# Optimization experiments

Hardware: AMD Instinct MI355X
Metric: run time of the kernel (lower is better)

The kernel has to match this reference:

```python
import jax, jax.numpy as jnp
import numpy as np

N_NODES = 50000
N_EDGES = 500000
D = 128
K_CLUSTERS = 1024  # fixed cluster count for Kongming_Cluster
EPS = 1e-8


def setup_inputs() -> dict:
    key = jax.random.key(0)
    k1, k2, k3, k4 = jax.random.split(key, 4)
    x = jax.random.normal(k1, (N_NODES, D), dtype=jnp.float32)
    edge_index = jax.random.randint(k2, (2, N_EDGES), 0, N_NODES, dtype=jnp.int32)
    W1 = jax.random.normal(k3, (D, D), dtype=jnp.float32) * (1.0 / np.sqrt(D))
    b1 = jax.random.normal(k4, (D,), dtype=jnp.float32) * 0.01
    return {"x": x, "edge_index": edge_index, "W1": W1, "b1": b1}


def reference(x, edge_index, W1, b1):
    src, dst = edge_index[0], edge_index[1]
    # --- SLPropagate: mean aggregation of neighbor features over edge list ---
    msg = x[src]                                               # [E, D] gather
    agg = jax.ops.segment_sum(msg, dst, num_segments=N_NODES)  # [N, D] scatter-add
    deg = jax.ops.segment_sum(jnp.ones((N_EDGES,), x.dtype), dst, num_segments=N_NODES)
    h = agg / jnp.maximum(deg, 1.0)[:, None]                   # [N, D]

    # --- Kongming_Cluster: cosine-similarity assignment to K centroids ---
    hn = h / (jnp.linalg.norm(h, axis=-1, keepdims=True) + EPS)  # row-normalized
    centroids = hn[:K_CLUSTERS]                                  # [K, D]
    sim = hn @ centroids.T                                       # [N, K] cosine sims
    assign = jnp.argmax(sim, axis=-1)                            # [N] cluster index
    counts = jax.ops.segment_sum(jnp.ones((N_NODES,), x.dtype), assign,
                                 num_segments=K_CLUSTERS)
    xc = jax.ops.segment_sum(h, assign, num_segments=K_CLUSTERS)
    xc = xc / jnp.maximum(counts, 1.0)[:, None]                  # [K, D] cluster means

    # --- lin1 on compressed representation ---
    y = xc @ W1.T + b1                                           # [K, D]

    # --- Kongming_Reconstruct: scatter/gather back to per-node rows ---
    out = y[assign]                                              # [N, D]
    return out
```

## Files before the change

### kernel.cpp

```cpp
#include <hip/hip_runtime.h>

#define N_NODES 50000
#define N_EDGES 500000
#define DIM 128
#define KC 1024
#define CAP 64
#define EPSV 1e-8f
#define LO_SCALE 4096.0f
#define INV_LO_SCALE (1.0f / 4096.0f)

typedef _Float16 f16x8 __attribute__((ext_vector_type(8)));
typedef _Float16 f16x2 __attribute__((ext_vector_type(2)));
typedef float f32x4 __attribute__((ext_vector_type(4)));

__global__ void fill_buckets_k(const int* __restrict__ ei, int* __restrict__ bucket,
                               int* __restrict__ cursor) {
    int e = blockIdx.x * blockDim.x + threadIdx.x;
    if (e >= N_EDGES) return;
    int src = ei[e];
    int dst = ei[N_EDGES + e];
    int pos = atomicAdd(cursor + dst, 1);
    if (pos < CAP) bucket[dst * CAP + pos] = src;
}

__global__ void agg_norm_k(const float* __restrict__ x, const int* __restrict__ bucket,
                           const int* __restrict__ cursor, float* __restrict__ h,
                           _Float16* __restrict__ Ahi, _Float16* __restrict__ Alo) {
    int lane = threadIdx.x & 63;
    int wv = threadIdx.x >> 6;
    int n = blockIdx.x * 4 + wv;

    int cnt = cursor[n];
    if (cnt > CAP) cnt = CAP;
    int v = (lane < cnt) ? bucket[n * CAP + lane] : 0x7fffffff;

#pragma unroll
    for (int k = 2; k <= 64; k <<= 1) {
#pragma unroll
        for (int j = k >> 1; j >= 1; j >>= 1) {
            int other = __shfl_xor(v, j);
            bool lower = ((lane & j) == 0);
            bool asc = ((lane & k) == 0);
            int mn = min(v, other), mx = max(v, other);
            v = (lower == asc) ? mn : mx;
        }
    }

    const float2* x2 = (const float2*)x;
    float ax = 0.f, ay = 0.f;
    for (int j = 0; j < cnt; ++j) {
        int s = __shfl(v, j);
        float2 t = x2[(size_t)s * 64 + lane];
        ax += t.x; ay += t.y;
    }
    float degf = (float)(cnt > 0 ? cnt : 1);
    float hx = ax / degf, hy = ay / degf;

    float ss = hx * hx + hy * hy;
#pragma unroll
    for (int o = 1; o < 64; o <<= 1) ss += __shfl_xor(ss, o);
    float denom = sqrtf(ss) + EPSV;
    float hnx = hx / denom, hny = hy / denom;

    ((float2*)h)[(size_t)n * 64 + lane] = make_float2(hx, hy);

    _Float16 hix = (_Float16)hnx, hiy = (_Float16)hny;
    _Float16 lox = (_Float16)((hnx - (float)hix) * LO_SCALE);
    _Float16 loy = (_Float16)((hny - (float)hiy) * LO_SCALE);
    f16x2 ph; ph[0] = hix; ph[1] = hiy;
    f16x2 pl; pl[0] = lox; pl[1] = loy;
    *(f16x2*)(Ahi + (size_t)n * DIM + lane * 2) = ph;
    *(f16x2*)(Alo + (size_t)n * DIM + lane * 2) = pl;
}

#define SWZ14(u) ((u) ^ ((((u) >> 8) & 7) << 4))

__global__ __launch_bounds__(256, 3) void sim_mfma3_k(const _Float16* __restrict__ Ahi,
                                                      const _Float16* __restrict__ Alo,
                                                      int* __restrict__ assign) {
    __shared__ __align__(16) char Bs[2][16384];
    const int lane = threadIdx.x & 63;
    const int wv = threadIdx.x >> 6;
    const int r16 = lane & 15, kg = lane >> 4;
    const int m0 = blockIdx.x * 128 + wv * 32;

    int ar0 = m0 + r16;      if (ar0 > N_NODES - 1) ar0 = N_NODES - 1;
    int ar1 = m0 + 16 + r16; if (ar1 > N_NODES - 1) ar1 = N_NODES - 1;
    f16x8 ah0[4], al0[4], ah1[4], al1[4];
#pragma unroll
    for (int ks = 0; ks < 4; ++ks) {
        size_t o0 = (size_t)ar0 * DIM + ks * 32 + kg * 8;
        size_t o1 = (size_t)ar1 * DIM + ks * 32 + kg * 8;
        ah0[ks] = *(const f16x8*)(Ahi + o0);
        al0[ks] = *(const f16x8*)(Alo + o0);
        ah1[ks] = *(const f16x8*)(Ahi + o1);
        al1[ks] = *(const f16x8*)(Alo + o1);
    }

    const int u0 = wv * 2048 + lane * 16;
    const int u1 = u0 + 1024;
    const int d0 = SWZ14(u0), d1 = SWZ14(u1);
    const int e0 = u0 >> 1, e1 = u1 >> 1;

    float best0_0 = -1e30f, best0_1 = -1e30f, best0_2 = -1e30f, best0_3 = -1e30f;
    float best1_0 = -1e30f, best1_1 = -1e30f, best1_2 = -1e30f, best1_3 = -1e30f;
    int bi0_0 = 0, bi0_1 = 0, bi0_2 = 0, bi0_3 = 0;
    int bi1_0 = 0, bi1_1 = 0, bi1_2 = 0, bi1_3 = 0;

    const int rbase = r16 * 256;
    const int x4 = (r16 & 7) << 4;

    f16x8 sA = *(const f16x8*)(Ahi + e0);
    f16x8 sB = *(const f16x8*)(Ahi + e1);
    f16x8 sC = *(const f16x8*)(Alo + e0);
    f16x8 sD = *(const f16x8*)(Alo + e1);
    {
        char* bc = &Bs[0][0];
        *(f16x8*)(bc + d0) = sA; *(f16x8*)(bc + d1) = sB;
        *(f16x8*)(bc + 8192 + d0) = sC; *(f16x8*)(bc + 8192 + d1) = sD;
    }
    __syncthreads();

    for (int kc = 0; kc < 32; ++kc) {
        const int cur = kc & 1;
        if (kc < 31) {
            int go = (kc + 1) * 4096;
            sA = *(const f16x8*)(Ahi + go + e0);
            sB = *(const f16x8*)(Ahi + go + e1);
            sC = *(const f16x8*)(Alo + go + e0);
            sD = *(const f16x8*)(Alo + go + e1);
        }
        char* bc = &Bs[cur][0];
#pragma unroll
        for (int ns = 0; ns < 2; ++ns) {
            f32x4 c1a = (f32x4){0.f, 0.f, 0.f, 0.f};
            f32x4 c2a = (f32x4){0.f, 0.f, 0.f, 0.f};
            f32x4 c1b = (f32x4){0.f, 0.f, 0.f, 0.f};
            f32x4 c2b = (f32x4){0.f, 0.f, 0.f, 0.f};
#pragma unroll
            for (int ks = 0; ks < 4; ++ks) {
                int off = ns * 4096 + rbase + ((ks * 64 + kg * 16) ^ x4);
                f16x8 bh = *(const f16x8*)(bc + off);
                f16x8 bl = *(const f16x8*)(bc + 8192 + off);
                c1a = __builtin_amdgcn_mfma_f32_16x16x32_f16(ah0[ks], bh, c1a, 0, 0, 0);
                c2a = __builtin_amdgcn_mfma_f32_16x16x32_f16(ah0[ks], bl, c2a, 0, 0, 0);
                c2a = __builtin_amdgcn_mfma_f32_16x16x32_f16(al0[ks], bh, c2a, 0, 0, 0);
                c1b = __builtin_amdgcn_mfma_f32_16x16x32_f16(ah1[ks], bh, c1b, 0, 0, 0);
                c2b = __builtin_amdgcn_mfma_f32_16x16x32_f16(ah1[ks], bl, c2b, 0, 0, 0);
                c2b = __builtin_amdgcn_mfma_f32_16x16x32_f16(al1[ks], bh, c2b, 0, 0, 0);
            }
            int col = kc * 32 + ns * 16 + r16;
            float s;
            s = c1a[0] + c2a[0] * INV_LO_SCALE; if (s > best0_0) { best0_0 = s; bi0_0 = col; }
            s = c1a[1] + c2a[1] * INV_LO_SCALE; if (s > best0_1) { best0_1 = s; bi0_1 = col; }
            s = c1a[2] + c2a[2] * INV_LO_SCALE; if (s > best0_2) { best0_2 = s; bi0_2 = col; }
            s = c1a[3] + c2a[3] * INV_LO_SCALE; if (s > best0_3) { best0_3 = s; bi0_3 = col; }
            s = c1b[0] + c2b[0] * INV_LO_SCALE; if (s > best1_0) { best1_0 = s; bi1_0 = col; }
            s = c1b[1] + c2b[1] * INV_LO_SCALE; if (s > best1_1) { best1_1 = s; bi1_1 = col; }
            s = c1b[2] + c2b[2] * INV_LO_SCALE; if (s > best1_2) { best1_2 = s; bi1_2 = col; }
            s = c1b[3] + c2b[3] * INV_LO_SCALE; if (s > best1_3) { best1_3 = s; bi1_3 = col; }
        }
        if (kc < 31) {
            char* bn = &Bs[cur ^ 1][0];
            *(f16x8*)(bn + d0) = sA; *(f16x8*)(bn + d1) = sB;
            *(f16x8*)(bn + 8192 + d0) = sC; *(f16x8*)(bn + 8192 + d1) = sD;
        }
        __syncthreads();
    }

    float bestA[8] = {best0_0, best0_1, best0_2, best0_3,
                      best1_0, best1_1, best1_2, best1_3};
    int bidxA[8] = {bi0_0, bi0_1, bi0_2, bi0_3, bi1_0, bi1_1, bi1_2, bi1_3};
#pragma unroll
    for (int q = 0; q < 8; ++q) {
        float b = bestA[q];
        int bi = bidxA[q];
#pragma unroll
        for (int o = 1; o < 16; o <<= 1) {
            float os = __shfl_xor(b, o);
            int oi = __shfl_xor(bi, o);
            if (os > b || (os == b && oi < bi)) { b = os; bi = oi; }
        }
        if (r16 == 0) {
            int gr = m0 + (q >> 2) * 16 + kg * 4 + (q & 3);
            if (gr < N_NODES) assign[gr] = bi;
        }
    }
}

__global__ void cluster_count_k(const int* __restrict__ assign, int* __restrict__ counts) {
    int n = blockIdx.x * 256 + threadIdx.x;
    if (n < N_NODES) atomicAdd(counts + assign[n], 1);
}

__global__ void scan_k(const int* __restrict__ counts, int* __restrict__ offs,
                       int* __restrict__ ccur) {
    __shared__ int buf[KC];
    int t = threadIdx.x;
    int v = counts[t];
    buf[t] = v;
    __syncthreads();
#pragma unroll
    for (int o = 1; o < KC; o <<= 1) {
        int u = (t >= o) ? buf[t - o] : 0;
        __syncthreads();
        buf[t] += u;
        __syncthreads();
    }
    int excl = buf[t] - v;
    offs[t] = excl;
    ccur[t] = excl;
}

__global__ void fill_clist_k(const int* __restrict__ assign, int* __restrict__ ccur,
                             int* __restrict__ clist) {
    int n = blockIdx.x * 256 + threadIdx.x;
    if (n >= N_NODES) return;
    int p = atomicAdd(ccur + assign[n], 1);
    clist[p] = n;
}

__global__ void xc_sum_k(const float* __restrict__ h, const int* __restrict__ clist,
                         const int* __restrict__ offs, const int* __restrict__ counts,
                         float* __restrict__ xc) {
    int c = blockIdx.x, t = threadIdx.x;
    int s = offs[c], cnt = counts[c];
    float acc = 0.f;
    for (int i = 0; i < cnt; ++i) {
        int n = clist[s + i];
        acc += h[(size_t)n * DIM + t];
    }
    xc[c * DIM + t] = acc;
}

__global__ void y_gemm_k(const float* __restrict__ xc, const int* __restrict__ counts,
                         const float* __restrict__ W1, const float* __restrict__ b1,
                         float* __restrict__ y) {
    __shared__ float xr[DIM];
    int c = blockIdx.x, t = threadIdx.x;
    int cnt = counts[c];
    float cntf = (float)(cnt > 0 ? cnt : 1);
    xr[t] = xc[c * DIM + t] / cntf;
    __syncthreads();

    const float4* w4 = (const float4*)(W1 + t * DIM);
    float a0 = 0.f, a1 = 0.f, a2 = 0.f, a3 = 0.f;
#pragma unroll
    for (int kk = 0; kk < 32; ++kk) {
        float4 w = w4[kk];
        a0 = fmaf(xr[4 * kk + 0], w.x, a0);
        a1 = fmaf(xr[4 * kk + 1], w.y, a1);
        a2 = fmaf(xr[4 * kk + 2], w.z, a2);
        a3 = fmaf(xr[4 * kk + 3], w.w, a3);
    }
    y[c * DIM + t] = (a0 + a1) + (a2 + a3) + b1[t];
}

__global__ void scatter_out_k(const float* __restrict__ y, const int* __restrict__ assign,
                              float* __restrict__ out) {
    int i = blockIdx.x * blockDim.x + threadIdx.x;
    int n = i >> 5, q = i & 31;
    int a = assign[n];
    ((float4*)out)[(size_t)n * 32 + q] = ((const float4*)y)[a * 32 + q];
}

extern "C" void kernel_launch(void* const* d_in, const int* in_sizes, int n_in,
                              void* d_out, int out_size, void* d_ws, size_t ws_size,
                              hipStream_t stream) {
    const float* x  = (const float*)d_in[0];
    const int*   ei = (const int*)d_in[1];
    const float* W1 = (const float*)d_in[2];
    const float* b1 = (const float*)d_in[3];
    float* out = (float*)d_out;

    char* ws = (char*)d_ws;
    float* h      = (float*)(ws);
    int*   bucket = (int*)(ws + 25600000);
    int*   clist  = (int*)(ws + 25600000);
    int*   offs   = (int*)(ws + 25800000);
    int*   ccur   = (int*)(ws + 25804096);
    int*   cursor = (int*)(ws + 38400000);
    int*   counts = (int*)(ws + 38600000);
    float* xc     = (float*)(ws + 38604096);
    int*   assign = (int*)(ws + 39128384);
    float* y      = (float*)(ws + 39328384);

    _Float16* Ahi = (_Float16*)d_out;
    _Float16* Alo = (_Float16*)((char*)d_out + 12800000);

    hipMemsetAsync(ws + 38400000, 0, 204096, stream);

    fill_buckets_k<<<(N_EDGES + 255) / 256, 256, 0, stream>>>(ei, bucket, cursor);
    agg_norm_k<<<N_NODES / 4, 256, 0, stream>>>(x, bucket, cursor, h, Ahi, Alo);
    sim_mfma3_k<<<(N_NODES + 127) / 128, 256, 0, stream>>>(Ahi, Alo, assign);
    cluster_count_k<<<(N_NODES + 255) / 256, 256, 0, stream>>>(assign, counts);
    scan_k<<<1, KC, 0, stream>>>(counts, offs, ccur);
    fill_clist_k<<<(N_NODES + 255) / 256, 256, 0, stream>>>(assign, ccur, clist);
    xc_sum_k<<<KC, 128, 0, stream>>>(h, clist, offs, counts, xc);
    y_gemm_k<<<KC, 128, 0, stream>>>(xc, counts, W1, b1, y);
    scatter_out_k<<<(N_NODES * 32) / 256, 256, 0, stream>>>(y, assign, out);
}
```

Baseline: 195.7 us.

## Process two nodes per wave in aggregation and fuse cluster counting and GEMM kernels

The aggregation kernel now handles two nodes per wavefront, with 32 lanes each loading float4 rows, whenever both degrees are at most 32. It falls back to the old one-node-per-wave path otherwise. Cluster counting is folded into the similarity kernel's argmax epilogue as atomics, and the cluster-sum and lin1 GEMM kernels are merged into one. This removes two kernel launches and one global xc round trip, and improves lane use for the typical degree of about 10. In exchange it adds a divergent fallback branch and atomic contention on the counts array.

```diff
diff --git a/kernel.cpp b/kernel.cpp
--- a/kernel.cpp
+++ b/kernel.cpp
@@ -10,6 +10,7 @@
 #define INV_LO_SCALE (1.0f / 4096.0f)
 
 typedef _Float16 f16x8 __attribute__((ext_vector_type(8)));
+typedef _Float16 f16x4 __attribute__((ext_vector_type(4)));
 typedef _Float16 f16x2 __attribute__((ext_vector_type(2)));
 typedef float f32x4 __attribute__((ext_vector_type(4)));
 
@@ -26,58 +27,112 @@
 __global__ void agg_norm_k(const float* __restrict__ x, const int* __restrict__ bucket,
                            const int* __restrict__ cursor, float* __restrict__ h,
                            _Float16* __restrict__ Ahi, _Float16* __restrict__ Alo) {
-    int lane = threadIdx.x & 63;
-    int wv = threadIdx.x >> 6;
-    int n = blockIdx.x * 4 + wv;
-
-    int cnt = cursor[n];
-    if (cnt > CAP) cnt = CAP;
-    int v = (lane < cnt) ? bucket[n * CAP + lane] : 0x7fffffff;
-
-#pragma unroll
-    for (int k = 2; k <= 64; k <<= 1) {
-#pragma unroll
-        for (int j = k >> 1; j >= 1; j >>= 1) {
-            int other = __shfl_xor(v, j);
-            bool lower = ((lane & j) == 0);
-            bool asc = ((lane & k) == 0);
-            int mn = min(v, other), mx = max(v, other);
-            v = (lower == asc) ? mn : mx;
-        }
-    }
-
-    const float2* x2 = (const float2*)x;
-    float ax = 0.f, ay = 0.f;
-    for (int j = 0; j < cnt; ++j) {
-        int s = __shfl(v, j);
-        float2 t = x2[(size_t)s * 64 + lane];
-        ax += t.x; ay += t.y;
-    }
-    float degf = (float)(cnt > 0 ? cnt : 1);
-    float hx = ax / degf, hy = ay / degf;
-
-    float ss = hx * hx + hy * hy;
-#pragma unroll
-    for (int o = 1; o < 64; o <<= 1) ss += __shfl_xor(ss, o);
-    float denom = sqrtf(ss) + EPSV;
-    float hnx = hx / denom, hny = hy / denom;
-
-    ((float2*)h)[(size_t)n * 64 + lane] = make_float2(hx, hy);
-
-    _Float16 hix = (_Float16)hnx, hiy = (_Float16)hny;
-    _Float16 lox = (_Float16)((hnx - (float)hix) * LO_SCALE);
-    _Float16 loy = (_Float16)((hny - (float)hiy) * LO_SCALE);
-    f16x2 ph; ph[0] = hix; ph[1] = hiy;
-    f16x2 pl; pl[0] = lox; pl[1] = loy;
-    *(f16x2*)(Ahi + (size_t)n * DIM + lane * 2) = ph;
-    *(f16x2*)(Alo + (size_t)n * DIM + lane * 2) = pl;
+    const int lane = threadIdx.x & 63;
+    const int wv = threadIdx.x >> 6;
+    const int half = lane >> 5, q = lane & 31;
+    const int n = blockIdx.x * 8 + wv * 2 + half;
+
+    int cnt_mine = cursor[n];
+    if (cnt_mine > CAP) cnt_mine = CAP;
+    int cnt_other = __shfl_xor(cnt_mine, 32);
+    int cmax = max(cnt_mine, cnt_other);
+
+    if (cmax <= 32) {
+        int v = (q < cnt_mine) ? bucket[n * CAP + q] : 0x7fffffff;
+#pragma unroll
+        for (int k = 2; k <= 32; k <<= 1) {
+#pragma unroll
+            for (int j = k >> 1; j >= 1; j >>= 1) {
+                int other = __shfl_xor(v, j);
+                bool lower = ((q & j) == 0);
+                bool asc = ((q & k) == 0);
+                int mn = min(v, other), mx = max(v, other);
+                v = (lower == asc) ? mn : mx;
+            }
+        }
+        const float4* x4p = (const float4*)x;
+        float4 a4 = make_float4(0.f, 0.f, 0.f, 0.f);
+        const int base = half << 5;
+        for (int j = 0; j < cmax; j += 2) {
+            int s0 = __shfl(v, base + j);
+            int s1 = __shfl(v, base + j + 1);
+            if (j < cnt_mine) {
+                float4 t = x4p[(size_t)s0 * 32 + q];
+                a4.x += t.x; a4.y += t.y; a4.z += t.z; a4.w += t.w;
+            }
+            if (j + 1 < cnt_mine) {
+                float4 t = x4p[(size_t)s1 * 32 + q];
+                a4.x += t.x; a4.y += t.y; a4.z += t.z; a4.w += t.w;
+            }
+        }
+        float inv = 1.0f / (float)(cnt_mine > 0 ? cnt_mine : 1);
+        float4 h4;
+        h4.x = a4.x * inv; h4.y = a4.y * inv; h4.z = a4.z * inv; h4.w = a4.w * inv;
+        float ss = h4.x * h4.x + h4.y * h4.y + h4.z * h4.z + h4.w * h4.w;
+#pragma unroll
+        for (int o = 1; o < 32; o <<= 1) ss += __shfl_xor(ss, o);
+        float sc = 1.0f / (sqrtf(ss) + EPSV);
+        float4 hn4;
+        hn4.x = h4.x * sc; hn4.y = h4.y * sc; hn4.z = h4.z * sc; hn4.w = h4.w * sc;
+
+        ((float4*)h)[(size_t)n * 32 + q] = h4;
+        _Float16 h0 = (_Float16)hn4.x, h1 = (_Float16)hn4.y;
+        _Float16 h2 = (_Float16)hn4.z, h3 = (_Float16)hn4.w;
+        f16x4 ph = {h0, h1, h2, h3};
+        f16x4 pl = {(_Float16)((hn4.x - (float)h0) * LO_SCALE),
+                    (_Float16)((hn4.y - (float)h1) * LO_SCALE),
+                    (_Float16)((hn4.z - (float)h2) * LO_SCALE),
+                    (_Float16)((hn4.w - (float)h3) * LO_SCALE)};
+        *(f16x4*)(Ahi + (size_t)n * DIM + q * 4) = ph;
+        *(f16x4*)(Alo + (size_t)n * DIM + q * 4) = pl;
+    } else {
+        for (int tt = 0; tt < 2; ++tt) {
+            int nn = blockIdx.x * 8 + wv * 2 + tt;
+            int cnt = cursor[nn];
+            if (cnt > CAP) cnt = CAP;
+            int v = (lane < cnt) ? bucket[nn * CAP + lane] : 0x7fffffff;
+#pragma unroll
+            for (int k = 2; k <= 64; k <<= 1) {
+#pragma unroll
+                for (int j = k >> 1; j >= 1; j >>= 1) {
+                    int other = __shfl_xor(v, j);
+                    bool lower = ((lane & j) == 0);
+                    bool asc = ((lane & k) == 0);
+                    int mn = min(v, other), mx = max(v, other);
+                    v = (lower == asc) ? mn : mx;
+                }
+            }
+            const float2* x2 = (const float2*)x;
+            float ax = 0.f, ay = 0.f;
+            for (int j = 0; j < cnt; ++j) {
+                int s = __shfl(v, j);
+                float2 t = x2[(size_t)s * 64 + lane];
+                ax += t.x; ay += t.y;
+            }
+            float degf = (float)(cnt > 0 ? cnt : 1);
+            float hx = ax / degf, hy = ay / degf;
+            float ss = hx * hx + hy * hy;
+#pragma unroll
+            for (int o = 1; o < 64; o <<= 1) ss += __shfl_xor(ss, o);
+            float denom = sqrtf(ss) + EPSV;
+            float hnx = hx / denom, hny = hy / denom;
+            ((float2*)h)[(size_t)nn * 64 + lane] = make_float2(hx, hy);
+            _Float16 hix = (_Float16)hnx, hiy = (_Float16)hny;
+            f16x2 ph; ph[0] = hix; ph[1] = hiy;
+            f16x2 pl; pl[0] = (_Float16)((hnx - (float)hix) * LO_SCALE);
+            pl[1] = (_Float16)((hny - (float)hiy) * LO_SCALE);
+            *(f16x2*)(Ahi + (size_t)nn * DIM + lane * 2) = ph;
+            *(f16x2*)(Alo + (size_t)nn * DIM + lane * 2) = pl;
+        }
+    }
 }
 
 #define SWZ14(u) ((u) ^ ((((u) >> 8) & 7) << 4))
 
 __global__ __launch_bounds__(256, 3) void sim_mfma3_k(const _Float16* __restrict__ Ahi,
                                                       const _Float16* __restrict__ Alo,
-                                                      int* __restrict__ assign) {
+                                                      int* __restrict__ assign,
+                                                      int* __restrict__ counts) {
     __shared__ __align__(16) char Bs[2][16384];
     const int lane = threadIdx.x & 63;
     const int wv = threadIdx.x >> 6;
@@ -172,9 +227,9 @@
                       best1_0, best1_1, best1_2, best1_3};
     int bidxA[8] = {bi0_0, bi0_1, bi0_2, bi0_3, bi1_0, bi1_1, bi1_2, bi1_3};
 #pragma unroll
-    for (int q = 0; q < 8; ++q) {
-        float b = bestA[q];
-        int bi = bidxA[q];
+    for (int qq = 0; qq < 8; ++qq) {
+        float b = bestA[qq];
+        int bi = bidxA[qq];
 #pragma unroll
         for (int o = 1; o < 16; o <<= 1) {
             float os = __shfl_xor(b, o);
@@ -182,15 +237,13 @@
             if (os > b || (os == b && oi < bi)) { b = os; bi = oi; }
         }
         if (r16 == 0) {
-            int gr = m0 + (q >> 2) * 16 + kg * 4 + (q & 3);
-            if (gr < N_NODES) assign[gr] = bi;
-        }
-    }
-}
-
-__global__ void cluster_count_k(const int* __restrict__ assign, int* __restrict__ counts) {
-    int n = blockIdx.x * 256 + threadIdx.x;
-    if (n < N_NODES) atomicAdd(counts + assign[n], 1);
+            int gr = m0 + (qq >> 2) * 16 + kg * 4 + (qq & 3);
+            if (gr < N_NODES) {
+                assign[gr] = bi;
+                atomicAdd(counts + bi, 1);
+            }
+        }
+    }
 }
 
 __global__ void scan_k(const int* __restrict__ counts, int* __restrict__ offs,
@@ -220,9 +273,11 @@
     clist[p] = n;
 }
 
-__global__ void xc_sum_k(const float* __restrict__ h, const int* __restrict__ clist,
-                         const int* __restrict__ offs, const int* __restrict__ counts,
-                         float* __restrict__ xc) {
+__global__ void xcy_k(const float* __restrict__ h, const int* __restrict__ clist,
+                      const int* __restrict__ offs, const int* __restrict__ counts,
+                      const float* __restrict__ W1, const float* __restrict__ b1,
+                      float* __restrict__ y) {
+    __shared__ float xr[DIM];
     int c = blockIdx.x, t = threadIdx.x;
     int s = offs[c], cnt = counts[c];
     float acc = 0.f;
@@ -230,17 +285,7 @@
         int n = clist[s + i];
         acc += h[(size_t)n * DIM + t];
     }
-    xc[c * DIM + t] = acc;
-}
-
-__global__ void y_gemm_k(const float* __restrict__ xc, const int* __restrict__ counts,
-                         const float* __restrict__ W1, const float* __restrict__ b1,
-                         float* __restrict__ y) {
-    __shared__ float xr[DIM];
-    int c = blockIdx.x, t = threadIdx.x;
-    int cnt = counts[c];
-    float cntf = (float)(cnt > 0 ? cnt : 1);
-    xr[t] = xc[c * DIM + t] / cntf;
+    xr[t] = acc / (float)(cnt > 0 ? cnt : 1);
     __syncthreads();
 
     const float4* w4 = (const float4*)(W1 + t * DIM);
@@ -281,7 +326,6 @@
     int*   ccur   = (int*)(ws + 25804096);
     int*   cursor = (int*)(ws + 38400000);
     int*   counts = (int*)(ws + 38600000);
-    float* xc     = (float*)(ws + 38604096);
     int*   assign = (int*)(ws + 39128384);
     float* y      = (float*)(ws + 39328384);
 
@@ -291,12 +335,10 @@
     hipMemsetAsync(ws + 38400000, 0, 204096, stream);
 
     fill_buckets_k<<<(N_EDGES + 255) / 256, 256, 0, stream>>>(ei, bucket, cursor);
-    agg_norm_k<<<N_NODES / 4, 256, 0, stream>>>(x, bucket, cursor, h, Ahi, Alo);
-    sim_mfma3_k<<<(N_NODES + 127) / 128, 256, 0, stream>>>(Ahi, Alo, assign);
-    cluster_count_k<<<(N_NODES + 255) / 256, 256, 0, stream>>>(assign, counts);
+    agg_norm_k<<<N_NODES / 8, 256, 0, stream>>>(x, bucket, cursor, h, Ahi, Alo);
+    sim_mfma3_k<<<(N_NODES + 127) / 128, 256, 0, stream>>>(Ahi, Alo, assign, counts);
     scan_k<<<1, KC, 0, stream>>>(counts, offs, ccur);
     fill_clist_k<<<(N_NODES + 255) / 256, 256, 0, stream>>>(assign, ccur, clist);
-    xc_sum_k<<<KC, 128, 0, stream>>>(h, clist, offs, counts, xc);
-    y_gemm_k<<<KC, 128, 0, stream>>>(xc, counts, W1, b1, y);
+    xcy_k<<<KC, 128, 0, stream>>>(h, clist, offs, counts, W1, b1, y);
     scatter_out_k<<<(N_NODES * 32) / 256, 256, 0, stream>>>(y, assign, out);
 }
```

New measurement: 179.7 us. 1.09x faster.
